# Optimization experiments

Measured on AMD Instinct MI355X. Metric: run time of the kernel, lower is better.

Reference implementation:

```python
import jax, jax.numpy as jnp
import numpy as np

COORD_DIM = 4
HIDDEN = 256
N_HIDDEN_LAYERS = 4  # num_layers - 1 hidden->hidden layers after the first
MIN_OMEGA = 10.0
MAX_OMEGA = 100.0
MEDIAN_OMEGA = (MIN_OMEGA + MAX_OMEGA) / 2.0
N = 524288


def _uniform(key, shape, bound):
    return jax.random.uniform(key, shape, jnp.float32, -bound, bound)


def setup_inputs() -> dict:
    key = jax.random.key(0)
    ks = jax.random.split(key, 16)
    coords = jax.random.normal(ks[0], (N, COORD_DIM), jnp.float32)
    # omega predictor: Linear(4, 64) -> ReLU -> Linear(64, 1) -> Sigmoid
    ow1 = _uniform(ks[1], (COORD_DIM, HIDDEN // 4), 1.0 / np.sqrt(COORD_DIM))
    ob1 = _uniform(ks[2], (HIDDEN // 4,), 1.0 / np.sqrt(COORD_DIM))
    ow2 = _uniform(ks[3], (HIDDEN // 4, 1), 1.0 / np.sqrt(HIDDEN // 4))
    ob2 = _uniform(ks[4], (1,), 1.0 / np.sqrt(HIDDEN // 4))
    # SIREN first layer: uniform(-1/in_features, 1/in_features)
    w0 = _uniform(ks[5], (COORD_DIM, HIDDEN), 1.0 / COORD_DIM)
    b0 = _uniform(ks[6], (HIDDEN,), 1.0 / np.sqrt(COORD_DIM))
    # SIREN hidden layers: uniform(-sqrt(6/in)/omega0, ...), stacked [4, 256, 256]
    hb = np.sqrt(6.0 / HIDDEN) / MEDIAN_OMEGA
    wh = _uniform(ks[7], (N_HIDDEN_LAYERS, HIDDEN, HIDDEN), hb)
    bh = _uniform(ks[8], (N_HIDDEN_LAYERS, HIDDEN), 1.0 / np.sqrt(HIDDEN))
    wf = _uniform(ks[9], (HIDDEN, 1), hb)
    bf = _uniform(ks[10], (1,), 1.0 / np.sqrt(HIDDEN))
    return {"coords": coords, "ow1": ow1, "ob1": ob1, "ow2": ow2, "ob2": ob2,
            "w0": w0, "b0": b0, "wh": wh, "bh": bh, "wf": wf, "bf": bf}


def reference(coords, ow1, ob1, ow2, ob2, w0, b0, wh, bh, wf, bf):
    # adaptive omega per coordinate: [N, 1]
    h = jax.nn.relu(coords @ ow1 + ob1)
    omega = MIN_OMEGA + (MAX_OMEGA - MIN_OMEGA) * jax.nn.sigmoid(h @ ow2 + ob2)
    # SIREN stack: x = sin(omega * (x @ W + b))
    x = jnp.sin(omega * (coords @ w0 + b0))
    for i in range(N_HIDDEN_LAYERS):
        x = jnp.sin(omega * (x @ wh[i] + bh[i]))
    return x @ wf + bf  # [N, 1]
```

## Files before the change

kernel.cpp:

```cpp
#include <hip/hip_runtime.h>
#include <hip/hip_bf16.h>

typedef _Float16 f16;
typedef f16 f16x4 __attribute__((ext_vector_type(4)));
typedef f16 f16x8 __attribute__((ext_vector_type(8)));
typedef __fp16 h16x2 __attribute__((ext_vector_type(2)));
typedef __fp16 h16x4 __attribute__((ext_vector_type(4)));
typedef float f32x4 __attribute__((ext_vector_type(4)));
typedef float f32x16 __attribute__((ext_vector_type(16)));

#define MT 128
#define LDST 260
#define INV2PI 0.15915494309189535f

__global__ __launch_bounds__(64)
void prep_wt(const float* __restrict__ wh, f16* __restrict__ wt) {
    const int b = blockIdx.x;
    const int layer = b >> 7, wcblk = (b >> 4) & 7, kblk = b & 15;
    const int lane = threadIdx.x;
    const int l31 = lane & 31, lh = lane >> 5;
    const float* src = wh + layer * 65536 + (kblk * 16 + lh * 8) * 256 + wcblk * 32 + l31;
    f16x8 v;
#pragma unroll
    for (int j = 0; j < 8; j++) v[j] = (f16)src[j * 256];
    *(f16x8*)(wt + b * 512 + lane * 8) = v;
}

__device__ inline f16x8 lds_ld8(const f16* p) {
    f16x4 lo = *(const f16x4*)p;
    f16x4 hi = *(const f16x4*)(p + 4);
    return __builtin_shufflevector(lo, hi, 0, 1, 2, 3, 4, 5, 6, 7);
}

__device__ inline f16x4 pk4(float z0, float z1, float z2, float z3) {
    h16x2 a = __builtin_amdgcn_cvt_pkrtz(z0, z1);
    h16x2 b = __builtin_amdgcn_cvt_pkrtz(z2, z3);
    h16x4 r = __builtin_shufflevector(a, b, 0, 1, 2, 3);
    return __builtin_bit_cast(f16x4, r);
}

__global__ __launch_bounds__(512, 4)
void siren_fused(const float* __restrict__ coords,
                 const float* __restrict__ ow1, const float* __restrict__ ob1,
                 const float* __restrict__ ow2, const float* __restrict__ ob2,
                 const float* __restrict__ w0, const float* __restrict__ b0,
                 const f16* __restrict__ wt,
                 const float* __restrict__ bh,
                 const float* __restrict__ wf,
                 const float* __restrict__ bf,
                 float* __restrict__ out) {
    __shared__ __align__(16) f16 Xs[MT * LDST];
    __shared__ float om_rev[MT];
    __shared__ __align__(16) float crd[MT * 4];
    __shared__ __align__(16) float bh_s[256];
    __shared__ __align__(16) float wf_s[256];

    const int t = threadIdx.x;
    const long base_pt = (long)blockIdx.x * MT;

    if (t < MT) ((f32x4*)crd)[t] = ((const f32x4*)(coords + base_pt * 4))[t];
    if (t < 256) wf_s[t] = wf[t];
    __syncthreads();

    if (t < MT) {
        const float c0 = crd[t * 4], c1 = crd[t * 4 + 1], c2 = crd[t * 4 + 2], c3 = crd[t * 4 + 3];
        float h[64];
#pragma unroll
        for (int j = 0; j < 64; j++) {
            float z = ob1[j] + c0 * ow1[j] + c1 * ow1[64 + j] + c2 * ow1[128 + j] + c3 * ow1[192 + j];
            h[j] = fmaxf(z, 0.f);
        }
        float z2 = ob2[0];
#pragma unroll
        for (int j = 0; j < 64; j++) z2 += h[j] * ow2[j];
        const float sig = 1.f / (1.f + __expf(-z2));
        om_rev[t] = (10.f + 90.f * sig) * INV2PI;
    }
    __syncthreads();

    {
        const int pt = t >> 2;
        const int q = t & 3;
        const float c0 = crd[pt * 4], c1 = crd[pt * 4 + 1], c2 = crd[pt * 4 + 2], c3 = crd[pt * 4 + 3];
        const float orv = om_rev[pt];
#pragma unroll
        for (int i = 0; i < 4; i++) {
            const int ch = (q + 4 * i) * 16;
#pragma unroll
            for (int c = 0; c < 16; c += 4) {
                f32x4 wv0 = *(const f32x4*)(w0 + 0 * 256 + ch + c);
                f32x4 wv1 = *(const f32x4*)(w0 + 1 * 256 + ch + c);
                f32x4 wv2 = *(const f32x4*)(w0 + 2 * 256 + ch + c);
                f32x4 wv3 = *(const f32x4*)(w0 + 3 * 256 + ch + c);
                f32x4 bv  = *(const f32x4*)(b0 + ch + c);
                float z[4];
#pragma unroll
                for (int j = 0; j < 4; j++) {
                    float zz = bv[j] + c0 * wv0[j] + c1 * wv1[j] + c2 * wv2[j] + c3 * wv3[j];
                    z[j] = __builtin_amdgcn_sinf(orv * zz);
                }
                *(f16x4*)&Xs[pt * LDST + ch + c] = pk4(z[0], z[1], z[2], z[3]);
            }
        }
    }
    __syncthreads();

    const int lane = t & 63;
    const int wave = t >> 6;
    const int l31 = lane & 31;
    const int lh = lane >> 5;
    const int wcg = wave & 3;
    const int pr0 = (wave >> 2) * 64;
    const int wc0 = wcg * 64;

    for (int layer = 0; layer < 4; layer++) {
        if (t < 256) bh_s[t] = bh[layer * 256 + t];

        const f16* afrag = wt + ((layer * 8 + wcg * 2) * 16) * 512 + lane * 8;
        const f16* bptr = &Xs[(pr0 + l31) * LDST + lh * 8];

        f32x16 acc[2][2];
#pragma unroll
        for (int ct = 0; ct < 2; ct++)
#pragma unroll
            for (int rt = 0; rt < 2; rt++)
#pragma unroll
                for (int j = 0; j < 16; j++) acc[ct][rt][j] = 0.f;

        f16x8 a0[3], a1[3];
#pragma unroll
        for (int d = 0; d < 3; d++) {
            a0[d] = *(const f16x8*)(afrag + d * 512);
            a1[d] = *(const f16x8*)(afrag + 8192 + d * 512);
        }

#pragma unroll
        for (int kb = 0; kb < 16; kb++) {
            const int s = kb % 3;
            f16x8 av0 = a0[s], av1 = a1[s];
            if (kb + 3 < 16) {
                a0[s] = *(const f16x8*)(afrag + (kb + 3) * 512);
                a1[s] = *(const f16x8*)(afrag + 8192 + (kb + 3) * 512);
            }
            f16x8 bv0 = lds_ld8(bptr + 0 * 32 * LDST + kb * 16);
            f16x8 bv1 = lds_ld8(bptr + 1 * 32 * LDST + kb * 16);
            acc[0][0] = __builtin_amdgcn_mfma_f32_32x32x16_f16(av0, bv0, acc[0][0], 0, 0, 0);
            acc[0][1] = __builtin_amdgcn_mfma_f32_32x32x16_f16(av0, bv1, acc[0][1], 0, 0, 0);
            acc[1][0] = __builtin_amdgcn_mfma_f32_32x32x16_f16(av1, bv0, acc[1][0], 0, 0, 0);
            acc[1][1] = __builtin_amdgcn_mfma_f32_32x32x16_f16(av1, bv1, acc[1][1], 0, 0, 0);
        }
        __syncthreads();

        float orv[2];
#pragma unroll
        for (int rt = 0; rt < 2; rt++) orv[rt] = om_rev[pr0 + rt * 32 + l31];
#pragma unroll
        for (int ct = 0; ct < 2; ct++) {
#pragma unroll
            for (int g = 0; g < 4; g++) {
                const int wc = wc0 + ct * 32 + g * 8 + lh * 4;
                f32x4 bb = *(const f32x4*)&bh_s[wc];
#pragma unroll
                for (int rt = 0; rt < 2; rt++) {
                    const int prow = pr0 + rt * 32 + l31;
                    float z[4];
#pragma unroll
                    for (int j = 0; j < 4; j++)
                        z[j] = __builtin_amdgcn_sinf(orv[rt] * (acc[ct][rt][g * 4 + j] + bb[j]));
                    *(f16x4*)&Xs[prow * LDST + wc] = pk4(z[0], z[1], z[2], z[3]);
                }
            }
        }
        __syncthreads();
    }

    {
        const int pt = t >> 2;
        const int q = t & 3;
        const f16* xrow = &Xs[pt * LDST];
        float s = 0.f;
#pragma unroll
        for (int i = 0; i < 4; i++) {
            const int ch = (q + 4 * i) * 16;
#pragma unroll
            for (int c = 0; c < 16; c += 4) {
                f16x4 xv = *(const f16x4*)(xrow + ch + c);
                f32x4 wv = *(const f32x4*)&wf_s[ch + c];
                s += (float)xv[0] * wv[0] + (float)xv[1] * wv[1]
                   + (float)xv[2] * wv[2] + (float)xv[3] * wv[3];
            }
        }
        s += __shfl_xor(s, 1, 64);
        s += __shfl_xor(s, 2, 64);
        if (q == 0) out[base_pt + pt] = s + bf[0];
    }
}

extern "C" void kernel_launch(void* const* d_in, const int* in_sizes, int n_in,
                              void* d_out, int out_size, void* d_ws, size_t ws_size,
                              hipStream_t stream) {
    (void)in_sizes; (void)n_in; (void)out_size; (void)ws_size;
    const float* coords = (const float*)d_in[0];
    const float* ow1 = (const float*)d_in[1];
    const float* ob1 = (const float*)d_in[2];
    const float* ow2 = (const float*)d_in[3];
    const float* ob2 = (const float*)d_in[4];
    const float* w0  = (const float*)d_in[5];
    const float* b0  = (const float*)d_in[6];
    const float* wh  = (const float*)d_in[7];
    const float* bh  = (const float*)d_in[8];
    const float* wf  = (const float*)d_in[9];
    const float* bf  = (const float*)d_in[10];
    float* out = (float*)d_out;
    f16* wt = (f16*)d_ws;

    prep_wt<<<512, 64, 0, stream>>>(wh, wt);
    siren_fused<<<524288 / MT, 512, 0, stream>>>(coords, ow1, ob1, ow2, ob2,
                                                 w0, b0, wt, bh, wf, bf, out);
}
```

Before: 450.5 us.

## Shrink tile to 64 points, fold omega into activations, prefetch weights across layers

Halves the point tile to 64 rows with 256 threads, so each wave covers all rows for its column group. The per-row omega scale is folded into the stored activations and the bias-initialised accumulators, which removes the add and multiply before each sine. All biases are preloaded once, and the weight-fragment prefetch now runs across layer boundaries so the next layer's first fragments are already in flight. The trade-offs are that each weight fragment is reused over fewer rows, and storing omega-scaled values in fp16 changes the rounding.

```diff
diff --git a/kernel.cpp b/kernel.cpp
--- a/kernel.cpp
+++ b/kernel.cpp
@@ -9,7 +9,7 @@
 typedef float f32x4 __attribute__((ext_vector_type(4)));
 typedef float f32x16 __attribute__((ext_vector_type(16)));
 
-#define MT 128
+#define MT 64
 #define LDST 260
 #define INV2PI 0.15915494309189535f
 
@@ -39,7 +39,7 @@
     return __builtin_bit_cast(f16x4, r);
 }
 
-__global__ __launch_bounds__(512, 4)
+__global__ __launch_bounds__(256, 4)
 void siren_fused(const float* __restrict__ coords,
                  const float* __restrict__ ow1, const float* __restrict__ ob1,
                  const float* __restrict__ ow2, const float* __restrict__ ob2,
@@ -52,14 +52,16 @@
     __shared__ __align__(16) f16 Xs[MT * LDST];
     __shared__ float om_rev[MT];
     __shared__ __align__(16) float crd[MT * 4];
-    __shared__ __align__(16) float bh_s[256];
+    __shared__ __align__(16) float bh_all[1024];
     __shared__ __align__(16) float wf_s[256];
 
     const int t = threadIdx.x;
     const long base_pt = (long)blockIdx.x * MT;
 
     if (t < MT) ((f32x4*)crd)[t] = ((const f32x4*)(coords + base_pt * 4))[t];
-    if (t < 256) wf_s[t] = wf[t];
+    wf_s[t] = wf[t];
+#pragma unroll
+    for (int i = 0; i < 4; i++) bh_all[t + 256 * i] = bh[t + 256 * i];
     __syncthreads();
 
     if (t < MT) {
@@ -97,7 +99,7 @@
 #pragma unroll
                 for (int j = 0; j < 4; j++) {
                     float zz = bv[j] + c0 * wv0[j] + c1 * wv1[j] + c2 * wv2[j] + c3 * wv3[j];
-                    z[j] = __builtin_amdgcn_sinf(orv * zz);
+                    z[j] = orv * __builtin_amdgcn_sinf(orv * zz);
                 }
                 *(f16x4*)&Xs[pt * LDST + ch + c] = pk4(z[0], z[1], z[2], z[3]);
             }
@@ -106,44 +108,53 @@
     __syncthreads();
 
     const int lane = t & 63;
-    const int wave = t >> 6;
+    const int wcg = t >> 6;
     const int l31 = lane & 31;
     const int lh = lane >> 5;
-    const int wcg = wave & 3;
-    const int pr0 = (wave >> 2) * 64;
     const int wc0 = wcg * 64;
 
+    const f16* bptr = &Xs[l31 * LDST + lh * 8];
+    float orv[2];
+#pragma unroll
+    for (int rt = 0; rt < 2; rt++) orv[rt] = om_rev[rt * 32 + l31];
+
+    const f16* afrag0 = wt + ((0 * 8 + wcg * 2) * 16) * 512 + lane * 8;
+    f16x8 a0[4], a1[4];
+#pragma unroll
+    for (int d = 0; d < 4; d++) {
+        a0[d] = *(const f16x8*)(afrag0 + d * 512);
+        a1[d] = *(const f16x8*)(afrag0 + 8192 + d * 512);
+    }
+
+#pragma unroll
     for (int layer = 0; layer < 4; layer++) {
-        if (t < 256) bh_s[t] = bh[layer * 256 + t];
-
         const f16* afrag = wt + ((layer * 8 + wcg * 2) * 16) * 512 + lane * 8;
-        const f16* bptr = &Xs[(pr0 + l31) * LDST + lh * 8];
+        const int next_off = (layer < 3) ? 65536 : -3 * 65536;
+        const float* bhl = bh_all + layer * 256;
 
         f32x16 acc[2][2];
 #pragma unroll
         for (int ct = 0; ct < 2; ct++)
 #pragma unroll
-            for (int rt = 0; rt < 2; rt++)
-#pragma unroll
-                for (int j = 0; j < 16; j++) acc[ct][rt][j] = 0.f;
-
-        f16x8 a0[3], a1[3];
-#pragma unroll
-        for (int d = 0; d < 3; d++) {
-            a0[d] = *(const f16x8*)(afrag + d * 512);
-            a1[d] = *(const f16x8*)(afrag + 8192 + d * 512);
-        }
+            for (int g = 0; g < 4; g++) {
+                const int wc = wc0 + ct * 32 + g * 8 + lh * 4;
+                f32x4 bb = *(const f32x4*)&bhl[wc];
+#pragma unroll
+                for (int rt = 0; rt < 2; rt++)
+#pragma unroll
+                    for (int j = 0; j < 4; j++) acc[ct][rt][g * 4 + j] = orv[rt] * bb[j];
+            }
 
 #pragma unroll
         for (int kb = 0; kb < 16; kb++) {
-            const int s = kb % 3;
+            const int s = kb & 3;
             f16x8 av0 = a0[s], av1 = a1[s];
-            if (kb + 3 < 16) {
-                a0[s] = *(const f16x8*)(afrag + (kb + 3) * 512);
-                a1[s] = *(const f16x8*)(afrag + 8192 + (kb + 3) * 512);
-            }
-            f16x8 bv0 = lds_ld8(bptr + 0 * 32 * LDST + kb * 16);
-            f16x8 bv1 = lds_ld8(bptr + 1 * 32 * LDST + kb * 16);
+            const int idx = kb + 4;
+            const f16* rb = afrag + (idx >= 16 ? next_off : 0) + (idx & 15) * 512;
+            a0[s] = *(const f16x8*)rb;
+            a1[s] = *(const f16x8*)(rb + 8192);
+            f16x8 bv0 = lds_ld8(bptr + kb * 16);
+            f16x8 bv1 = lds_ld8(bptr + 32 * LDST + kb * 16);
             acc[0][0] = __builtin_amdgcn_mfma_f32_32x32x16_f16(av0, bv0, acc[0][0], 0, 0, 0);
             acc[0][1] = __builtin_amdgcn_mfma_f32_32x32x16_f16(av0, bv1, acc[0][1], 0, 0, 0);
             acc[1][0] = __builtin_amdgcn_mfma_f32_32x32x16_f16(av1, bv0, acc[1][0], 0, 0, 0);
@@ -151,22 +162,20 @@
         }
         __syncthreads();
 
-        float orv[2];
-#pragma unroll
-        for (int rt = 0; rt < 2; rt++) orv[rt] = om_rev[pr0 + rt * 32 + l31];
 #pragma unroll
         for (int ct = 0; ct < 2; ct++) {
 #pragma unroll
             for (int g = 0; g < 4; g++) {
                 const int wc = wc0 + ct * 32 + g * 8 + lh * 4;
-                f32x4 bb = *(const f32x4*)&bh_s[wc];
 #pragma unroll
                 for (int rt = 0; rt < 2; rt++) {
-                    const int prow = pr0 + rt * 32 + l31;
+                    const int prow = rt * 32 + l31;
                     float z[4];
 #pragma unroll
-                    for (int j = 0; j < 4; j++)
-                        z[j] = __builtin_amdgcn_sinf(orv[rt] * (acc[ct][rt][g * 4 + j] + bb[j]));
+                    for (int j = 0; j < 4; j++) {
+                        float v = __builtin_amdgcn_sinf(acc[ct][rt][g * 4 + j]);
+                        z[j] = (layer < 3) ? orv[rt] * v : v;
+                    }
                     *(f16x4*)&Xs[prow * LDST + wc] = pk4(z[0], z[1], z[2], z[3]);
                 }
             }
@@ -215,6 +224,6 @@
     f16* wt = (f16*)d_ws;
 
     prep_wt<<<512, 64, 0, stream>>>(wh, wt);
-    siren_fused<<<524288 / MT, 512, 0, stream>>>(coords, ow1, ob1, ow2, ob2,
+    siren_fused<<<524288 / MT, 256, 0, stream>>>(coords, ow1, ob1, ow2, ob2,
                                                  w0, b0, wt, bh, wf, bf, out);
 }
```

New measurement: 466.4 us. 3.5% more time.
